# Optimization experiments

Hardware: AMD Instinct MI355X
Metric: run time of the kernel (lower is better)

The kernel has to match this reference:

```python
import jax, jax.numpy as jnp
import numpy as np

TEMPERATURE = 0.2
EPS = 1e-12  # matches torch F.normalize eps


def _l2_normalize(x):
    n = jnp.linalg.norm(x, axis=-1, keepdims=True)
    return x / jnp.maximum(n, EPS)


def setup_inputs() -> dict:
    key = jax.random.key(0)
    k1, k2 = jax.random.split(key)
    B, D = 8192, 256
    return {
        "user_embeddings": jax.random.normal(k1, (B, D), dtype=jnp.float32),
        "positive_item_embeddings": jax.random.normal(k2, (B, D), dtype=jnp.float32),
    }


def reference(user_embeddings, positive_item_embeddings):
    # all_item_embeddings=None branch: in-batch implicit negatives.
    u = _l2_normalize(user_embeddings)            # [B, D]
    p = _l2_normalize(positive_item_embeddings)   # [B, D]
    sim = jnp.einsum("bd,nd->bn", u, p) / TEMPERATURE  # [B, B]
    pos_sim = jnp.diagonal(sim)                   # [B]; equals the torch pos_sim
    # Original concatenates pos_sim[i] with the off-diagonal row entries and takes
    # logsumexp. Since the diagonal of sim IS pos_sim[i], that set equals the full
    # row, so loss_i = -pos_sim_i + logsumexp(sim[i, :]). Vectorized over the batch.
    lse = jax.nn.logsumexp(sim, axis=1)           # [B]
    return jnp.mean(lse - pos_sim)
```

## Files before the change

### kernel.cpp

```cpp
#include <hip/hip_runtime.h>
#include <hip/hip_bf16.h>

#define DDIM 256
#define NROWS 8192
#define LOG2E5 7.2134752044448170f

typedef __attribute__((ext_vector_type(8))) __bf16 bf16x8;
typedef __attribute__((ext_vector_type(4))) float floatx4;


__global__ __launch_bounds__(256) void normalize_repack(
    const float* __restrict__ U, const float* __restrict__ P,
    unsigned short* __restrict__ Af, unsigned short* __restrict__ Pf,
    float* __restrict__ possim, float* __restrict__ rowsum,
    float* __restrict__ out, int* __restrict__ counter)
{
    __shared__ unsigned short Ut[16 * 264];
    __shared__ unsigned short Pt[16 * 264];
    const int tid = threadIdx.x;
    const int R   = blockIdx.x;
    const int r16 = tid >> 4;
    const int c   = tid & 15;
    const int row = R * 16 + r16;

    if (R == 0 && tid == 0) { out[0] = 0.0f; counter[0] = 0; }
    if (c == 0) rowsum[row] = 0.0f;

    float4 u4[4], p4[4];
    float su = 0.0f, sp = 0.0f, up = 0.0f;
    #pragma unroll
    for (int j = 0; j < 4; ++j) {
        const size_t base = (size_t)row * DDIM + c * 16 + j * 4;
        u4[j] = *(const float4*)(U + base);
        p4[j] = *(const float4*)(P + base);
        su += u4[j].x*u4[j].x + u4[j].y*u4[j].y + u4[j].z*u4[j].z + u4[j].w*u4[j].w;
        sp += p4[j].x*p4[j].x + p4[j].y*p4[j].y + p4[j].z*p4[j].z + p4[j].w*p4[j].w;
        up += u4[j].x*p4[j].x + u4[j].y*p4[j].y + u4[j].z*p4[j].z + u4[j].w*p4[j].w;
    }
    #pragma unroll
    for (int d = 1; d < 16; d <<= 1) {
        su += __shfl_xor(su, d);
        sp += __shfl_xor(sp, d);
        up += __shfl_xor(up, d);
    }
    const float iu = rsqrtf(fmaxf(su, 1e-24f));
    const float ip = rsqrtf(fmaxf(sp, 1e-24f));
    if (c == 0) possim[row] = up * iu * ip;

    #pragma unroll
    for (int j = 0; j < 4; ++j) {
        union { ushort4 s4; __hip_bfloat16 h[4]; } cu, cp;
        cu.h[0] = __float2bfloat16(u4[j].x * iu); cu.h[1] = __float2bfloat16(u4[j].y * iu);
        cu.h[2] = __float2bfloat16(u4[j].z * iu); cu.h[3] = __float2bfloat16(u4[j].w * iu);
        cp.h[0] = __float2bfloat16(p4[j].x * ip); cp.h[1] = __float2bfloat16(p4[j].y * ip);
        cp.h[2] = __float2bfloat16(p4[j].z * ip); cp.h[3] = __float2bfloat16(p4[j].w * ip);
        *(ushort4*)&Ut[r16 * 264 + c * 16 + j * 4] = cu.s4;
        *(ushort4*)&Pt[r16 * 264 + c * 16 + j * 4] = cp.s4;
    }
    __syncthreads();

    const int lane = tid & 63;
    const int wv   = tid >> 6;
    const int m = lane & 15, q = lane >> 4;
    #pragma unroll
    for (int g = 0; g < 2; ++g) {
        const int G = wv * 2 + g;
        const bf16x8 ua = *(const bf16x8*)&Ut[m * 264 + G * 32 + q * 8];
        const bf16x8 pa = *(const bf16x8*)&Pt[m * 264 + G * 32 + q * 8];
        const size_t o = ((size_t)(R * 8 + G) * 64 + lane) * 8;
        *(bf16x8*)(Af + o) = ua;
        *(bf16x8*)(Pf + o) = pa;
    }
}

__global__ __launch_bounds__(256, 2) void sim_exp_rowsum(
    const unsigned short* __restrict__ Af,
    const unsigned short* __restrict__ Pf,
    float* __restrict__ rowsum,
    const float* __restrict__ possim,
    int* __restrict__ counter,
    float* __restrict__ out)
{
    __shared__ float ws4[4];
    __shared__ int ticket_s;
    const int tid  = threadIdx.x;
    const int lane = tid & 63;
    const int wv   = tid >> 6;
    const int wr   = wv >> 1, wc = wv & 1;
    const int m = lane & 15, q = lane >> 4;

    const int oct    = blockIdx.x & 7;
    const int stripe = blockIdx.x >> 3;

    bf16x8 afr[4][8];
    #pragma unroll
    for (int t = 0; t < 4; ++t)
        #pragma unroll
        for (int ks = 0; ks < 8; ++ks)
            afr[t][ks] = *(const bf16x8*)(Af +
                ((size_t)((stripe * 8 + wr * 4 + t) * 8 + ks) * 64 + lane) * 8);

    float rowpart[4][4];
    #pragma unroll
    for (int t = 0; t < 4; ++t)
        #pragma unroll
        for (int r = 0; r < 4; ++r)
            rowpart[t][r] = 0.0f;

    for (int i = 0; i < 16; ++i) {
        const int RB0 = oct * 64 + i * 4 + wc * 2;
        const unsigned short* B0 = Pf + ((size_t)RB0 * 8 * 64 + lane) * 8;

        floatx4 acc[4][2];
        #pragma unroll
        for (int t = 0; t < 4; ++t) {
            acc[t][0] = {0.0f, 0.0f, 0.0f, 0.0f};
            acc[t][1] = {0.0f, 0.0f, 0.0f, 0.0f};
        }
        #pragma unroll
        for (int ks = 0; ks < 8; ++ks) {
            const bf16x8 b0 = *(const bf16x8*)(B0 + (size_t)ks * 512);
            const bf16x8 b1 = *(const bf16x8*)(B0 + (size_t)(8 + ks) * 512);
            #pragma unroll
            for (int t = 0; t < 4; ++t) {
                acc[t][0] = __builtin_amdgcn_mfma_f32_16x16x32_bf16(
                    afr[t][ks], b0, acc[t][0], 0, 0, 0);
                acc[t][1] = __builtin_amdgcn_mfma_f32_16x16x32_bf16(
                    afr[t][ks], b1, acc[t][1], 0, 0, 0);
            }
        }
        #pragma unroll
        for (int t = 0; t < 4; ++t)
            #pragma unroll
            for (int r = 0; r < 4; ++r)
                rowpart[t][r] += exp2f(LOG2E5 * acc[t][0][r])
                               + exp2f(LOG2E5 * acc[t][1][r]);
    }

    #pragma unroll
    for (int t = 0; t < 4; ++t) {
        #pragma unroll
        for (int r = 0; r < 4; ++r) {
            float s = rowpart[t][r];
            s += __shfl_xor(s, 1);
            s += __shfl_xor(s, 2);
            s += __shfl_xor(s, 4);
            s += __shfl_xor(s, 8);
            if (m == 0) {
                const int grow = stripe * 128 + wr * 64 + t * 16 + q * 4 + r;
                atomicAdd(&rowsum[grow], s);
            }
        }
    }

    __threadfence();
    __syncthreads();
    if (tid == 0)
        ticket_s = __hip_atomic_fetch_add(counter, 1, __ATOMIC_ACQ_REL,
                                          __HIP_MEMORY_SCOPE_AGENT);
    __syncthreads();
    if (ticket_s == 511) {
        float part = 0.0f;
        for (int idx = tid; idx < NROWS; idx += 256) {
            const float rs = __hip_atomic_load(&rowsum[idx], __ATOMIC_RELAXED,
                                               __HIP_MEMORY_SCOPE_AGENT);
            part += __logf(rs) - 5.0f * possim[idx];
        }
        #pragma unroll
        for (int d = 1; d < 64; d <<= 1) part += __shfl_xor(part, d);
        if (lane == 0) ws4[wv] = part;
        __syncthreads();
        if (tid == 0)
            out[0] = (ws4[0] + ws4[1] + ws4[2] + ws4[3]) * (1.0f / (float)NROWS);
    }
}

extern "C" void kernel_launch(void* const* d_in, const int* in_sizes, int n_in,
                              void* d_out, int out_size, void* d_ws, size_t ws_size,
                              hipStream_t stream) {
    const float* U = (const float*)d_in[0];
    const float* P = (const float*)d_in[1];
    float* out = (float*)d_out;
    char* ws = (char*)d_ws;
    unsigned short* Af = (unsigned short*)ws;
    unsigned short* Pf = (unsigned short*)(ws + 4194304);
    float* rowsum = (float*)(ws + 8388608);
    float* possim = (float*)(ws + 8388608 + 32768);
    int* counter  = (int*)(ws + 8388608 + 65536);

    normalize_repack<<<NROWS / 16, 256, 0, stream>>>(U, P, Af, Pf, possim, rowsum,
                                                     out, counter);
    sim_exp_rowsum<<<512, 256, 0, stream>>>(Af, Pf, rowsum, possim, counter, out);
}
```

Before: 156.1 us.

## Switch to 32x32x16 MFMA with 128x128 output tiles and 4096 blocks

Repacks the normalized bf16 operands into the fragment layout of the 32x32x16 MFMA. The similarity kernel is restructured from 512 blocks, each streaming 16 column chunks against register-resident A fragments, into 4096 blocks that each compute one 128x128 tile with register double-buffered global loads. Blocks are remapped with XCD-aware swizzling and occupancy is raised to 4 blocks per CU. This trades A-fragment reuse across column tiles, which now means more global/L2 traffic, for larger MFMA tiles, more parallelism, and 8x more rowsum atomics.

```diff
diff --git a/kernel.cpp b/kernel.cpp
--- a/kernel.cpp
+++ b/kernel.cpp
@@ -5,8 +5,8 @@
 #define NROWS 8192
 #define LOG2E5 7.2134752044448170f
 
-typedef __attribute__((ext_vector_type(8))) __bf16 bf16x8;
-typedef __attribute__((ext_vector_type(4))) float floatx4;
+typedef __attribute__((ext_vector_type(8)))  __bf16 bf16x8;
+typedef __attribute__((ext_vector_type(16))) float  floatx16;
 
 
 __global__ __launch_bounds__(256) void normalize_repack(
@@ -15,22 +15,22 @@
     float* __restrict__ possim, float* __restrict__ rowsum,
     float* __restrict__ out, int* __restrict__ counter)
 {
-    __shared__ unsigned short Ut[16 * 264];
-    __shared__ unsigned short Pt[16 * 264];
+    __shared__ unsigned short Ut[32 * 264];
+    __shared__ unsigned short Pt[32 * 264];
     const int tid = threadIdx.x;
     const int R   = blockIdx.x;
-    const int r16 = tid >> 4;
-    const int c   = tid & 15;
-    const int row = R * 16 + r16;
+    const int r32 = tid >> 3;
+    const int c   = tid & 7;
+    const int row = R * 32 + r32;
 
     if (R == 0 && tid == 0) { out[0] = 0.0f; counter[0] = 0; }
     if (c == 0) rowsum[row] = 0.0f;
 
-    float4 u4[4], p4[4];
+    float4 u4[8], p4[8];
     float su = 0.0f, sp = 0.0f, up = 0.0f;
     #pragma unroll
-    for (int j = 0; j < 4; ++j) {
-        const size_t base = (size_t)row * DDIM + c * 16 + j * 4;
+    for (int j = 0; j < 8; ++j) {
+        const size_t base = (size_t)row * DDIM + c * 32 + j * 4;
         u4[j] = *(const float4*)(U + base);
         p4[j] = *(const float4*)(P + base);
         su += u4[j].x*u4[j].x + u4[j].y*u4[j].y + u4[j].z*u4[j].z + u4[j].w*u4[j].w;
@@ -38,7 +38,7 @@
         up += u4[j].x*p4[j].x + u4[j].y*p4[j].y + u4[j].z*p4[j].z + u4[j].w*p4[j].w;
     }
     #pragma unroll
-    for (int d = 1; d < 16; d <<= 1) {
+    for (int d = 1; d < 8; d <<= 1) {
         su += __shfl_xor(su, d);
         sp += __shfl_xor(sp, d);
         up += __shfl_xor(up, d);
@@ -48,32 +48,33 @@
     if (c == 0) possim[row] = up * iu * ip;
 
     #pragma unroll
-    for (int j = 0; j < 4; ++j) {
+    for (int j = 0; j < 8; ++j) {
         union { ushort4 s4; __hip_bfloat16 h[4]; } cu, cp;
         cu.h[0] = __float2bfloat16(u4[j].x * iu); cu.h[1] = __float2bfloat16(u4[j].y * iu);
         cu.h[2] = __float2bfloat16(u4[j].z * iu); cu.h[3] = __float2bfloat16(u4[j].w * iu);
         cp.h[0] = __float2bfloat16(p4[j].x * ip); cp.h[1] = __float2bfloat16(p4[j].y * ip);
         cp.h[2] = __float2bfloat16(p4[j].z * ip); cp.h[3] = __float2bfloat16(p4[j].w * ip);
-        *(ushort4*)&Ut[r16 * 264 + c * 16 + j * 4] = cu.s4;
-        *(ushort4*)&Pt[r16 * 264 + c * 16 + j * 4] = cp.s4;
+        *(ushort4*)&Ut[r32 * 264 + c * 32 + j * 4] = cu.s4;
+        *(ushort4*)&Pt[r32 * 264 + c * 32 + j * 4] = cp.s4;
     }
     __syncthreads();
 
     const int lane = tid & 63;
     const int wv   = tid >> 6;
-    const int m = lane & 15, q = lane >> 4;
+    const int m  = lane & 31;
+    const int kh = lane >> 5;
     #pragma unroll
-    for (int g = 0; g < 2; ++g) {
-        const int G = wv * 2 + g;
-        const bf16x8 ua = *(const bf16x8*)&Ut[m * 264 + G * 32 + q * 8];
-        const bf16x8 pa = *(const bf16x8*)&Pt[m * 264 + G * 32 + q * 8];
-        const size_t o = ((size_t)(R * 8 + G) * 64 + lane) * 8;
+    for (int g = 0; g < 4; ++g) {
+        const int G = wv * 4 + g;
+        const bf16x8 ua = *(const bf16x8*)&Ut[m * 264 + G * 16 + kh * 8];
+        const bf16x8 pa = *(const bf16x8*)&Pt[m * 264 + G * 16 + kh * 8];
+        const size_t o = ((size_t)(R * 16 + G) * 64 + lane) * 8;
         *(bf16x8*)(Af + o) = ua;
         *(bf16x8*)(Pf + o) = pa;
     }
 }
 
-__global__ __launch_bounds__(256, 2) void sim_exp_rowsum(
+__global__ __launch_bounds__(256, 4) void sim_exp_rowsum(
     const unsigned short* __restrict__ Af,
     const unsigned short* __restrict__ Pf,
     float* __restrict__ rowsum,
@@ -87,68 +88,61 @@
     const int lane = tid & 63;
     const int wv   = tid >> 6;
     const int wr   = wv >> 1, wc = wv & 1;
-    const int m = lane & 15, q = lane >> 4;
 
-    const int oct    = blockIdx.x & 7;
-    const int stripe = blockIdx.x >> 3;
+    const int xcd = blockIdx.x & 7;
+    const int lin = blockIdx.x >> 3;
+    const int CX  = xcd * 8 + (lin & 7);
+    const int RY  = lin >> 3;
 
-    bf16x8 afr[4][8];
+    const size_t abase = ((size_t)(RY * 4 + wr * 2) * 16 * 64 + lane) * 8;
+    const size_t bbase = ((size_t)(CX * 4 + wc * 2) * 16 * 64 + lane) * 8;
+
+    floatx16 acc[2][2];
     #pragma unroll
-    for (int t = 0; t < 4; ++t)
+    for (int t = 0; t < 2; ++t)
         #pragma unroll
-        for (int ks = 0; ks < 8; ++ks)
-            afr[t][ks] = *(const bf16x8*)(Af +
-                ((size_t)((stripe * 8 + wr * 4 + t) * 8 + ks) * 64 + lane) * 8);
+        for (int u = 0; u < 2; ++u)
+            #pragma unroll
+            for (int r = 0; r < 16; ++r)
+                acc[t][u][r] = 0.0f;
 
-    float rowpart[4][4];
+    bf16x8 a0 = *(const bf16x8*)(Af + abase);
+    bf16x8 a1 = *(const bf16x8*)(Af + abase + 8192);
+    bf16x8 b0 = *(const bf16x8*)(Pf + bbase);
+    bf16x8 b1 = *(const bf16x8*)(Pf + bbase + 8192);
+
     #pragma unroll
-    for (int t = 0; t < 4; ++t)
-        #pragma unroll
-        for (int r = 0; r < 4; ++r)
-            rowpart[t][r] = 0.0f;
-
-    for (int i = 0; i < 16; ++i) {
-        const int RB0 = oct * 64 + i * 4 + wc * 2;
-        const unsigned short* B0 = Pf + ((size_t)RB0 * 8 * 64 + lane) * 8;
-
-        floatx4 acc[4][2];
-        #pragma unroll
-        for (int t = 0; t < 4; ++t) {
-            acc[t][0] = {0.0f, 0.0f, 0.0f, 0.0f};
-            acc[t][1] = {0.0f, 0.0f, 0.0f, 0.0f};
+    for (int ks = 0; ks < 16; ++ks) {
+        bf16x8 a0n, a1n, b0n, b1n;
+        if (ks < 15) {
+            const size_t ko = (size_t)(ks + 1) * 512;
+            a0n = *(const bf16x8*)(Af + abase + ko);
+            a1n = *(const bf16x8*)(Af + abase + 8192 + ko);
+            b0n = *(const bf16x8*)(Pf + bbase + ko);
+            b1n = *(const bf16x8*)(Pf + bbase + 8192 + ko);
         }
-        #pragma unroll
-        for (int ks = 0; ks < 8; ++ks) {
-            const bf16x8 b0 = *(const bf16x8*)(B0 + (size_t)ks * 512);
-            const bf16x8 b1 = *(const bf16x8*)(B0 + (size_t)(8 + ks) * 512);
-            #pragma unroll
-            for (int t = 0; t < 4; ++t) {
-                acc[t][0] = __builtin_amdgcn_mfma_f32_16x16x32_bf16(
-                    afr[t][ks], b0, acc[t][0], 0, 0, 0);
-                acc[t][1] = __builtin_amdgcn_mfma_f32_16x16x32_bf16(
-                    afr[t][ks], b1, acc[t][1], 0, 0, 0);
-            }
-        }
-        #pragma unroll
-        for (int t = 0; t < 4; ++t)
-            #pragma unroll
-            for (int r = 0; r < 4; ++r)
-                rowpart[t][r] += exp2f(LOG2E5 * acc[t][0][r])
-                               + exp2f(LOG2E5 * acc[t][1][r]);
+        acc[0][0] = __builtin_amdgcn_mfma_f32_32x32x16_bf16(a0, b0, acc[0][0], 0, 0, 0);
+        acc[0][1] = __builtin_amdgcn_mfma_f32_32x32x16_bf16(a0, b1, acc[0][1], 0, 0, 0);
+        acc[1][0] = __builtin_amdgcn_mfma_f32_32x32x16_bf16(a1, b0, acc[1][0], 0, 0, 0);
+        acc[1][1] = __builtin_amdgcn_mfma_f32_32x32x16_bf16(a1, b1, acc[1][1], 0, 0, 0);
+        if (ks < 15) { a0 = a0n; a1 = a1n; b0 = b0n; b1 = b1n; }
     }
 
     #pragma unroll
-    for (int t = 0; t < 4; ++t) {
+    for (int t = 0; t < 2; ++t) {
         #pragma unroll
-        for (int r = 0; r < 4; ++r) {
-            float s = rowpart[t][r];
+        for (int reg = 0; reg < 16; ++reg) {
+            float s = exp2f(LOG2E5 * acc[t][0][reg])
+                    + exp2f(LOG2E5 * acc[t][1][reg]);
             s += __shfl_xor(s, 1);
             s += __shfl_xor(s, 2);
             s += __shfl_xor(s, 4);
             s += __shfl_xor(s, 8);
-            if (m == 0) {
-                const int grow = stripe * 128 + wr * 64 + t * 16 + q * 4 + r;
-                atomicAdd(&rowsum[grow], s);
+            s += __shfl_xor(s, 16);
+            if ((lane & 31) == 0) {
+                const int row = RY * 128 + wr * 64 + t * 32
+                              + (reg & 3) + 8 * (reg >> 2) + 4 * (lane >> 5);
+                atomicAdd(&rowsum[row], s);
             }
         }
     }
@@ -159,7 +153,7 @@
         ticket_s = __hip_atomic_fetch_add(counter, 1, __ATOMIC_ACQ_REL,
                                           __HIP_MEMORY_SCOPE_AGENT);
     __syncthreads();
-    if (ticket_s == 511) {
+    if (ticket_s == 4095) {
         float part = 0.0f;
         for (int idx = tid; idx < NROWS; idx += 256) {
             const float rs = __hip_atomic_load(&rowsum[idx], __ATOMIC_RELAXED,
@@ -188,7 +182,7 @@
     float* possim = (float*)(ws + 8388608 + 32768);
     int* counter  = (int*)(ws + 8388608 + 65536);
 
-    normalize_repack<<<NROWS / 16, 256, 0, stream>>>(U, P, Af, Pf, possim, rowsum,
+    normalize_repack<<<NROWS / 32, 256, 0, stream>>>(U, P, Af, Pf, possim, rowsum,
                                                      out, counter);
-    sim_exp_rowsum<<<512, 256, 0, stream>>>(Af, Pf, rowsum, possim, counter, out);
+    sim_exp_rowsum<<<4096, 256, 0, stream>>>(Af, Pf, rowsum, possim, counter, out);
 }
```

Result: slower. 494.6 us (+216.8%).

## Switch similarity GEMM to fp8 MFMA with per-block 128x128 output tiles

Applied to the files above, without the earlier changes.

Normalized embeddings are now quantized to fp8 (e4m3 via cvt_pk_fp8) instead of bf16, and the GEMM uses 16x16x32 fp8 MFMA, which halves operand bytes. The sim kernel is restructured from 512 blocks, each streaming 1024 columns with A kept in registers, to 4096 blocks that each compute one 128x128 tile with a double-buffered k-loop. The exp and row-sum run once at the end, followed by atomics into rowsum. This trades accuracy, since fp8 dot products of unit vectors scaled by 5 before exp may drift, for more MFMA throughput and parallelism, at the cost of 8x more atomics and more block launches.

```diff
diff --git a/kernel.cpp b/kernel.cpp
--- a/kernel.cpp
+++ b/kernel.cpp
@@ -1,29 +1,30 @@
 #include <hip/hip_runtime.h>
 #include <hip/hip_bf16.h>
+#include <stdint.h>
 
 #define DDIM 256
 #define NROWS 8192
 #define LOG2E5 7.2134752044448170f
 
-typedef __attribute__((ext_vector_type(8))) __bf16 bf16x8;
 typedef __attribute__((ext_vector_type(4))) float floatx4;
-
-
-__global__ __launch_bounds__(256) void normalize_repack(
+typedef __attribute__((ext_vector_type(2))) long longx2;
+
+
+__global__ __launch_bounds__(256) void normalize_repack_fp8(
     const float* __restrict__ U, const float* __restrict__ P,
-    unsigned short* __restrict__ Af, unsigned short* __restrict__ Pf,
+    unsigned char* __restrict__ Af, unsigned char* __restrict__ Pf,
     float* __restrict__ possim, float* __restrict__ rowsum,
     float* __restrict__ out, int* __restrict__ counter)
 {
-    __shared__ unsigned short Ut[16 * 264];
-    __shared__ unsigned short Pt[16 * 264];
+    __shared__ unsigned char Ut[16 * 272];
+    __shared__ unsigned char Pt[16 * 272];
     const int tid = threadIdx.x;
-    const int R   = blockIdx.x;
+    const int Rg  = blockIdx.x;
     const int r16 = tid >> 4;
     const int c   = tid & 15;
-    const int row = R * 16 + r16;
-
-    if (R == 0 && tid == 0) { out[0] = 0.0f; counter[0] = 0; }
+    const int row = Rg * 16 + r16;
+
+    if (Rg == 0 && tid == 0) { out[0] = 0.0f; counter[0] = 0; }
     if (c == 0) rowsum[row] = 0.0f;
 
     float4 u4[4], p4[4];
@@ -47,35 +48,39 @@
     const float ip = rsqrtf(fmaxf(sp, 1e-24f));
     if (c == 0) possim[row] = up * iu * ip;
 
+    int4 qu, qp;
+    int* quv = (int*)&qu; int* qpv = (int*)&qp;
     #pragma unroll
     for (int j = 0; j < 4; ++j) {
-        union { ushort4 s4; __hip_bfloat16 h[4]; } cu, cp;
-        cu.h[0] = __float2bfloat16(u4[j].x * iu); cu.h[1] = __float2bfloat16(u4[j].y * iu);
-        cu.h[2] = __float2bfloat16(u4[j].z * iu); cu.h[3] = __float2bfloat16(u4[j].w * iu);
-        cp.h[0] = __float2bfloat16(p4[j].x * ip); cp.h[1] = __float2bfloat16(p4[j].y * ip);
-        cp.h[2] = __float2bfloat16(p4[j].z * ip); cp.h[3] = __float2bfloat16(p4[j].w * ip);
-        *(ushort4*)&Ut[r16 * 264 + c * 16 + j * 4] = cu.s4;
-        *(ushort4*)&Pt[r16 * 264 + c * 16 + j * 4] = cp.s4;
-    }
+        int t;
+        t = __builtin_amdgcn_cvt_pk_fp8_f32(u4[j].x * iu, u4[j].y * iu, 0, false);
+        t = __builtin_amdgcn_cvt_pk_fp8_f32(u4[j].z * iu, u4[j].w * iu, t, true);
+        quv[j] = t;
+        t = __builtin_amdgcn_cvt_pk_fp8_f32(p4[j].x * ip, p4[j].y * ip, 0, false);
+        t = __builtin_amdgcn_cvt_pk_fp8_f32(p4[j].z * ip, p4[j].w * ip, t, true);
+        qpv[j] = t;
+    }
+    *(int4*)&Ut[r16 * 272 + c * 16] = qu;
+    *(int4*)&Pt[r16 * 272 + c * 16] = qp;
     __syncthreads();
 
     const int lane = tid & 63;
-    const int wv   = tid >> 6;
+    const int kp   = tid >> 6;
     const int m = lane & 15, q = lane >> 4;
-    #pragma unroll
-    for (int g = 0; g < 2; ++g) {
-        const int G = wv * 2 + g;
-        const bf16x8 ua = *(const bf16x8*)&Ut[m * 264 + G * 32 + q * 8];
-        const bf16x8 pa = *(const bf16x8*)&Pt[m * 264 + G * 32 + q * 8];
-        const size_t o = ((size_t)(R * 8 + G) * 64 + lane) * 8;
-        *(bf16x8*)(Af + o) = ua;
-        *(bf16x8*)(Pf + o) = pa;
-    }
+    const int lb = m * 272 + kp * 64 + q * 8;
+    int4 vu, vp;
+    *(int2*)&vu.x = *(const int2*)&Ut[lb];
+    *(int2*)&vu.z = *(const int2*)&Ut[lb + 32];
+    *(int2*)&vp.x = *(const int2*)&Pt[lb];
+    *(int2*)&vp.z = *(const int2*)&Pt[lb + 32];
+    const size_t o = (size_t)(Rg * 4 + kp) * 1024 + lane * 16;
+    *(int4*)(Af + o) = vu;
+    *(int4*)(Pf + o) = vp;
 }
 
-__global__ __launch_bounds__(256, 2) void sim_exp_rowsum(
-    const unsigned short* __restrict__ Af,
-    const unsigned short* __restrict__ Pf,
+__global__ __launch_bounds__(256) void sim_exp_rowsum(
+    const unsigned char* __restrict__ Af,
+    const unsigned char* __restrict__ Pf,
     float* __restrict__ rowsum,
     const float* __restrict__ possim,
     int* __restrict__ counter,
@@ -89,65 +94,68 @@
     const int wr   = wv >> 1, wc = wv & 1;
     const int m = lane & 15, q = lane >> 4;
 
-    const int oct    = blockIdx.x & 7;
-    const int stripe = blockIdx.x >> 3;
-
-    bf16x8 afr[4][8];
+    const int oct = blockIdx.x & 7;
+    const int lin = blockIdx.x >> 3;
+    const int CX  = oct * 8 + (lin & 7);
+    const int RY  = lin >> 3;
+
+    const unsigned char* Ab = Af + (size_t)(RY * 8 + wr * 4) * 4096 + lane * 16;
+    const unsigned char* Bb = Pf + (size_t)(CX * 8 + wc * 4) * 4096 + lane * 16;
+
+    floatx4 acc[4][4];
     #pragma unroll
     for (int t = 0; t < 4; ++t)
         #pragma unroll
-        for (int ks = 0; ks < 8; ++ks)
-            afr[t][ks] = *(const bf16x8*)(Af +
-                ((size_t)((stripe * 8 + wr * 4 + t) * 8 + ks) * 64 + lane) * 8);
-
-    float rowpart[4][4];
-    #pragma unroll
-    for (int t = 0; t < 4; ++t)
-        #pragma unroll
-        for (int r = 0; r < 4; ++r)
-            rowpart[t][r] = 0.0f;
-
-    for (int i = 0; i < 16; ++i) {
-        const int RB0 = oct * 64 + i * 4 + wc * 2;
-        const unsigned short* B0 = Pf + ((size_t)RB0 * 8 * 64 + lane) * 8;
-
-        floatx4 acc[4][2];
-        #pragma unroll
-        for (int t = 0; t < 4; ++t) {
-            acc[t][0] = {0.0f, 0.0f, 0.0f, 0.0f};
-            acc[t][1] = {0.0f, 0.0f, 0.0f, 0.0f};
-        }
-        #pragma unroll
-        for (int ks = 0; ks < 8; ++ks) {
-            const bf16x8 b0 = *(const bf16x8*)(B0 + (size_t)ks * 512);
-            const bf16x8 b1 = *(const bf16x8*)(B0 + (size_t)(8 + ks) * 512);
-            #pragma unroll
-            for (int t = 0; t < 4; ++t) {
-                acc[t][0] = __builtin_amdgcn_mfma_f32_16x16x32_bf16(
-                    afr[t][ks], b0, acc[t][0], 0, 0, 0);
-                acc[t][1] = __builtin_amdgcn_mfma_f32_16x16x32_bf16(
-                    afr[t][ks], b1, acc[t][1], 0, 0, 0);
-            }
+        for (int u = 0; u < 4; ++u)
+            acc[t][u] = {0.0f, 0.0f, 0.0f, 0.0f};
+
+    longx2 a[4], b[4];
+    #pragma unroll
+    for (int t = 0; t < 4; ++t) a[t] = *(const longx2*)(Ab + t * 4096);
+    #pragma unroll
+    for (int u = 0; u < 4; ++u) b[u] = *(const longx2*)(Bb + u * 4096);
+
+    #pragma unroll
+    for (int kp = 0; kp < 4; ++kp) {
+        longx2 an[4], bn[4];
+        if (kp < 3) {
+            #pragma unroll
+            for (int t = 0; t < 4; ++t)
+                an[t] = *(const longx2*)(Ab + t * 4096 + (kp + 1) * 1024);
+            #pragma unroll
+            for (int u = 0; u < 4; ++u)
+                bn[u] = *(const longx2*)(Bb + u * 4096 + (kp + 1) * 1024);
         }
         #pragma unroll
         for (int t = 0; t < 4; ++t)
             #pragma unroll
-            for (int r = 0; r < 4; ++r)
-                rowpart[t][r] += exp2f(LOG2E5 * acc[t][0][r])
-                               + exp2f(LOG2E5 * acc[t][1][r]);
+            for (int u = 0; u < 4; ++u)
+                acc[t][u] = __builtin_amdgcn_mfma_f32_16x16x32_fp8_fp8(
+                    a[t].x, b[u].x, acc[t][u], 0, 0, 0);
+        #pragma unroll
+        for (int t = 0; t < 4; ++t)
+            #pragma unroll
+            for (int u = 0; u < 4; ++u)
+                acc[t][u] = __builtin_amdgcn_mfma_f32_16x16x32_fp8_fp8(
+                    a[t].y, b[u].y, acc[t][u], 0, 0, 0);
+        if (kp < 3) {
+            #pragma unroll
+            for (int t = 0; t < 4; ++t) { a[t] = an[t]; b[t] = bn[t]; }
+        }
     }
 
     #pragma unroll
     for (int t = 0; t < 4; ++t) {
         #pragma unroll
         for (int r = 0; r < 4; ++r) {
-            float s = rowpart[t][r];
+            float s = exp2f(LOG2E5 * acc[t][0][r]) + exp2f(LOG2E5 * acc[t][1][r])
+                    + exp2f(LOG2E5 * acc[t][2][r]) + exp2f(LOG2E5 * acc[t][3][r]);
             s += __shfl_xor(s, 1);
             s += __shfl_xor(s, 2);
             s += __shfl_xor(s, 4);
             s += __shfl_xor(s, 8);
             if (m == 0) {
-                const int grow = stripe * 128 + wr * 64 + t * 16 + q * 4 + r;
+                const int grow = RY * 128 + wr * 64 + t * 16 + q * 4 + r;
                 atomicAdd(&rowsum[grow], s);
             }
         }
@@ -159,7 +167,7 @@
         ticket_s = __hip_atomic_fetch_add(counter, 1, __ATOMIC_ACQ_REL,
                                           __HIP_MEMORY_SCOPE_AGENT);
     __syncthreads();
-    if (ticket_s == 511) {
+    if (ticket_s == 4095) {
         float part = 0.0f;
         for (int idx = tid; idx < NROWS; idx += 256) {
             const float rs = __hip_atomic_load(&rowsum[idx], __ATOMIC_RELAXED,
@@ -182,13 +190,13 @@
     const float* P = (const float*)d_in[1];
     float* out = (float*)d_out;
     char* ws = (char*)d_ws;
-    unsigned short* Af = (unsigned short*)ws;
-    unsigned short* Pf = (unsigned short*)(ws + 4194304);
-    float* rowsum = (float*)(ws + 8388608);
-    float* possim = (float*)(ws + 8388608 + 32768);
-    int* counter  = (int*)(ws + 8388608 + 65536);
-
-    normalize_repack<<<NROWS / 16, 256, 0, stream>>>(U, P, Af, Pf, possim, rowsum,
-                                                     out, counter);
-    sim_exp_rowsum<<<512, 256, 0, stream>>>(Af, Pf, rowsum, possim, counter, out);
+    unsigned char* Af = (unsigned char*)ws;
+    unsigned char* Pf = (unsigned char*)(ws + 2097152);
+    float* rowsum = (float*)(ws + 4194304);
+    float* possim = (float*)(ws + 4194304 + 32768);
+    int* counter  = (int*)(ws + 4194304 + 65536);
+
+    normalize_repack_fp8<<<NROWS / 16, 256, 0, stream>>>(U, P, Af, Pf, possim,
+                                                         rowsum, out, counter);
+    sim_exp_rowsum<<<4096, 256, 0, stream>>>(Af, Pf, rowsum, possim, counter, out);
 }
```

New measurement: 416.2 us. 2.67x slower.

## Tile sim GEMM into 128x128 blocks with double-buffered async LDS staging

Applied to the files above, without the earlier changes.

Replaces the per-block 128-row stripe that held A fragments in registers and streamed B from global memory with a 4096-block grid of 128x128 output tiles. A and B are double-buffered in LDS through global_load_lds async copies over four K chunks, so each B fragment is shared across waves instead of being reloaded from global by each wave. The exp and row sum now run once per tile at the end. The cost is many more blocks, more rowsum atomics (8x), and 64KB of LDS per block, which limits occupancy.

```diff
diff --git a/kernel.cpp b/kernel.cpp
--- a/kernel.cpp
+++ b/kernel.cpp
@@ -7,6 +7,13 @@
 
 typedef __attribute__((ext_vector_type(8))) __bf16 bf16x8;
 typedef __attribute__((ext_vector_type(4))) float floatx4;
+
+__device__ __forceinline__ void async16(const void* g, void* l) {
+    __builtin_amdgcn_global_load_lds(
+        (const __attribute__((address_space(1))) unsigned int*)g,
+        (__attribute__((address_space(3))) unsigned int*)l,
+        16, 0, 0);
+}
 
 
 __global__ __launch_bounds__(256) void normalize_repack(
@@ -18,12 +25,12 @@
     __shared__ unsigned short Ut[16 * 264];
     __shared__ unsigned short Pt[16 * 264];
     const int tid = threadIdx.x;
-    const int R   = blockIdx.x;
+    const int Rg  = blockIdx.x;
     const int r16 = tid >> 4;
     const int c   = tid & 15;
-    const int row = R * 16 + r16;
-
-    if (R == 0 && tid == 0) { out[0] = 0.0f; counter[0] = 0; }
+    const int row = Rg * 16 + r16;
+
+    if (Rg == 0 && tid == 0) { out[0] = 0.0f; counter[0] = 0; }
     if (c == 0) rowsum[row] = 0.0f;
 
     float4 u4[4], p4[4];
@@ -67,13 +74,13 @@
         const int G = wv * 2 + g;
         const bf16x8 ua = *(const bf16x8*)&Ut[m * 264 + G * 32 + q * 8];
         const bf16x8 pa = *(const bf16x8*)&Pt[m * 264 + G * 32 + q * 8];
-        const size_t o = ((size_t)(R * 8 + G) * 64 + lane) * 8;
+        const size_t o = ((size_t)(Rg * 8 + G) * 64 + lane) * 8;
         *(bf16x8*)(Af + o) = ua;
         *(bf16x8*)(Pf + o) = pa;
     }
 }
 
-__global__ __launch_bounds__(256, 2) void sim_exp_rowsum(
+__global__ void sim_exp_rowsum(
     const unsigned short* __restrict__ Af,
     const unsigned short* __restrict__ Pf,
     float* __restrict__ rowsum,
@@ -81,73 +88,84 @@
     int* __restrict__ counter,
     float* __restrict__ out)
 {
+    __shared__ __align__(16) unsigned short Abuf[2][8192];
+    __shared__ __align__(16) unsigned short Bbuf[2][8192];
     __shared__ float ws4[4];
     __shared__ int ticket_s;
+
     const int tid  = threadIdx.x;
     const int lane = tid & 63;
     const int wv   = tid >> 6;
     const int wr   = wv >> 1, wc = wv & 1;
     const int m = lane & 15, q = lane >> 4;
 
-    const int oct    = blockIdx.x & 7;
-    const int stripe = blockIdx.x >> 3;
-
-    bf16x8 afr[4][8];
+    const int oct = blockIdx.x & 7;
+    const int lin = blockIdx.x >> 3;
+    const int CX  = oct * 8 + (lin & 7);
+    const int RY  = lin >> 3;
+
+    const unsigned char* Ag = (const unsigned char*)Af + (size_t)RY * 8 * 8192;
+    const unsigned char* Bg = (const unsigned char*)Pf + (size_t)CX * 8 * 8192;
+
+    auto stage = [&](int b, int kc) {
+        #pragma unroll
+        for (int j = 0; j < 4; ++j) {
+            const int blk = wv * 4 + j;
+            const int g   = blk >> 1;
+            const int gg  = blk & 1;
+            const size_t go = (size_t)g * 8192 + (size_t)(kc * 2 + gg) * 1024
+                            + (size_t)lane * 16;
+            async16(Ag + go, &Abuf[b][blk * 512]);
+            async16(Bg + go, &Bbuf[b][blk * 512]);
+        }
+    };
+
+    floatx4 acc[4][4];
     #pragma unroll
     for (int t = 0; t < 4; ++t)
         #pragma unroll
-        for (int ks = 0; ks < 8; ++ks)
-            afr[t][ks] = *(const bf16x8*)(Af +
-                ((size_t)((stripe * 8 + wr * 4 + t) * 8 + ks) * 64 + lane) * 8);
-
-    float rowpart[4][4];
-    #pragma unroll
-    for (int t = 0; t < 4; ++t)
-        #pragma unroll
-        for (int r = 0; r < 4; ++r)
-            rowpart[t][r] = 0.0f;
-
-    for (int i = 0; i < 16; ++i) {
-        const int RB0 = oct * 64 + i * 4 + wc * 2;
-        const unsigned short* B0 = Pf + ((size_t)RB0 * 8 * 64 + lane) * 8;
-
-        floatx4 acc[4][2];
-        #pragma unroll
-        for (int t = 0; t < 4; ++t) {
-            acc[t][0] = {0.0f, 0.0f, 0.0f, 0.0f};
-            acc[t][1] = {0.0f, 0.0f, 0.0f, 0.0f};
-        }
-        #pragma unroll
-        for (int ks = 0; ks < 8; ++ks) {
-            const bf16x8 b0 = *(const bf16x8*)(B0 + (size_t)ks * 512);
-            const bf16x8 b1 = *(const bf16x8*)(B0 + (size_t)(8 + ks) * 512);
+        for (int u = 0; u < 4; ++u)
+            acc[t][u] = {0.0f, 0.0f, 0.0f, 0.0f};
+
+    stage(0, 0);
+    __syncthreads();
+
+    #pragma unroll
+    for (int kc = 0; kc < 4; ++kc) {
+        if (kc < 3) stage((kc + 1) & 1, kc + 1);
+        const unsigned short* Ap = Abuf[kc & 1];
+        const unsigned short* Bp = Bbuf[kc & 1];
+        #pragma unroll
+        for (int ks = 0; ks < 2; ++ks) {
+            bf16x8 a[4], b[4];
             #pragma unroll
-            for (int t = 0; t < 4; ++t) {
-                acc[t][0] = __builtin_amdgcn_mfma_f32_16x16x32_bf16(
-                    afr[t][ks], b0, acc[t][0], 0, 0, 0);
-                acc[t][1] = __builtin_amdgcn_mfma_f32_16x16x32_bf16(
-                    afr[t][ks], b1, acc[t][1], 0, 0, 0);
-            }
-        }
-        #pragma unroll
-        for (int t = 0; t < 4; ++t)
+            for (int t = 0; t < 4; ++t)
+                a[t] = *(const bf16x8*)&Ap[((wr * 4 + t) * 2 + ks) * 512 + lane * 8];
             #pragma unroll
-            for (int r = 0; r < 4; ++r)
-                rowpart[t][r] += exp2f(LOG2E5 * acc[t][0][r])
-                               + exp2f(LOG2E5 * acc[t][1][r]);
+            for (int u = 0; u < 4; ++u)
+                b[u] = *(const bf16x8*)&Bp[((wc * 4 + u) * 2 + ks) * 512 + lane * 8];
+            #pragma unroll
+            for (int t = 0; t < 4; ++t)
+                #pragma unroll
+                for (int u = 0; u < 4; ++u)
+                    acc[t][u] = __builtin_amdgcn_mfma_f32_16x16x32_bf16(
+                        a[t], b[u], acc[t][u], 0, 0, 0);
+        }
+        if (kc < 3) __syncthreads();
     }
 
     #pragma unroll
     for (int t = 0; t < 4; ++t) {
         #pragma unroll
         for (int r = 0; r < 4; ++r) {
-            float s = rowpart[t][r];
+            float s = exp2f(LOG2E5 * acc[t][0][r]) + exp2f(LOG2E5 * acc[t][1][r])
+                    + exp2f(LOG2E5 * acc[t][2][r]) + exp2f(LOG2E5 * acc[t][3][r]);
             s += __shfl_xor(s, 1);
             s += __shfl_xor(s, 2);
             s += __shfl_xor(s, 4);
             s += __shfl_xor(s, 8);
             if (m == 0) {
-                const int grow = stripe * 128 + wr * 64 + t * 16 + q * 4 + r;
+                const int grow = RY * 128 + wr * 64 + t * 16 + q * 4 + r;
                 atomicAdd(&rowsum[grow], s);
             }
         }
@@ -159,7 +177,7 @@
         ticket_s = __hip_atomic_fetch_add(counter, 1, __ATOMIC_ACQ_REL,
                                           __HIP_MEMORY_SCOPE_AGENT);
     __syncthreads();
-    if (ticket_s == 511) {
+    if (ticket_s == 4095) {
         float part = 0.0f;
         for (int idx = tid; idx < NROWS; idx += 256) {
             const float rs = __hip_atomic_load(&rowsum[idx], __ATOMIC_RELAXED,
@@ -190,5 +208,5 @@
 
     normalize_repack<<<NROWS / 16, 256, 0, stream>>>(U, P, Af, Pf, possim, rowsum,
                                                      out, counter);
-    sim_exp_rowsum<<<512, 256, 0, stream>>>(Af, Pf, rowsum, possim, counter, out);
-}
+    sim_exp_rowsum<<<4096, 256, 0, stream>>>(Af, Pf, rowsum, possim, counter, out);
+}
```

New measurement: 446.0 us. +185.7%, slower.
